# Kernel tuning notes

Hardware: AMD Instinct MI355X
Metric: run time of the kernel (lower is better)

Reference implementation:

```python
import jax, jax.numpy as jnp
import numpy as np

EPS = 1e-6
SKEL_ITERS = 10

def _minpool(x, kh, kw):
    # torch: -max_pool2d(-x) pads with +inf for the min
    return jax.lax.reduce_window(x, jnp.inf, jax.lax.min,
                                 (1, 1, kh, kw), (1, 1, 1, 1),
                                 ((0, 0), (0, 0), (kh // 2, kh // 2), (kw // 2, kw // 2)))

def _maxpool3(x):
    return jax.lax.reduce_window(x, -jnp.inf, jax.lax.max,
                                 (1, 1, 3, 3), (1, 1, 1, 1),
                                 ((0, 0), (0, 0), (1, 1), (1, 1)))

def soft_erode(img):
    return jnp.minimum(_minpool(img, 3, 1), _minpool(img, 1, 3))

def soft_open(img):
    return _maxpool3(soft_erode(img))

def soft_skeletonize(img, iterations=SKEL_ITERS):
    img = jnp.clip(img, 0.0, 1.0)
    skeleton = jax.nn.relu(img - soft_open(img))
    for _ in range(iterations):
        img = soft_erode(img)
        delta = jax.nn.relu(img - soft_open(img))
        skeleton = skeleton + jax.nn.relu(delta - skeleton * delta)
    return jnp.clip(skeleton, 0.0, 1.0)

def _bce_with_logits(x, t):
    # numerically stable elementwise BCE
    return jnp.maximum(x, 0.0) - x * t + jnp.log1p(jnp.exp(-jnp.abs(x)))

def binary_focal_loss_with_logits(logits, target, alpha=0.25, gamma=2.0):
    bce = _bce_with_logits(logits, target)
    probs = jax.nn.sigmoid(logits)
    p_t = probs * target + (1.0 - probs) * (1.0 - target)
    alpha_t = alpha * target + (1.0 - alpha) * (1.0 - target)
    return jnp.mean(alpha_t * (1.0 - p_t) ** gamma * bce)

def dice_loss_from_probs(pred, target, eps=EPS):
    p = pred.reshape(pred.shape[0], -1)
    t = target.reshape(target.shape[0], -1)
    inter = jnp.sum(p * t, axis=1)
    denom = jnp.sum(p, axis=1) + jnp.sum(t, axis=1)
    dice = (2.0 * inter + eps) / (denom + eps)
    return 1.0 - jnp.mean(dice)

def cldice_loss(pred_probs, target_probs, iterations=SKEL_ITERS, eps=EPS):
    ps = soft_skeletonize(pred_probs, iterations)
    ts = soft_skeletonize(target_probs, iterations)
    B = pred_probs.shape[0]
    prec = jnp.sum((ps * target_probs).reshape(B, -1), axis=1) / (jnp.sum(ps.reshape(B, -1), axis=1) + eps)
    sens = jnp.sum((ts * pred_probs).reshape(B, -1), axis=1) / (jnp.sum(ts.reshape(B, -1), axis=1) + eps)
    cl = (2.0 * prec * sens + eps) / (prec + sens + eps)
    return 1.0 - jnp.mean(cl)

def masked_smooth_l1(pred, target, mask):
    m = jnp.broadcast_to(mask, pred.shape)
    d = pred * m - target * m
    ad = jnp.abs(d)
    sl1 = jnp.where(ad < 1.0, 0.5 * d * d, ad - 0.5)
    msum = jnp.sum(m)
    loss = jnp.sum(sl1) / jnp.maximum(msum, 1.0)
    return jnp.where(msum == 0.0, 0.0, loss)

def setup_inputs() -> dict:
    key = jax.random.key(0)
    ks = jax.random.split(key, 12)
    shp = (8, 1, 512, 512)
    ashp = (8, 2, 512, 512)
    return {
        'mask_logits': jax.random.normal(ks[0], shp, jnp.float32),
        'skeleton_logits': jax.random.normal(ks[1], shp, jnp.float32),
        'uncertainty_logits': jax.random.normal(ks[2], shp, jnp.float32),
        'junction_logits': jax.random.normal(ks[3], shp, jnp.float32),
        'endpoint_logits': jax.random.normal(ks[4], shp, jnp.float32),
        'affinity_pred': jax.random.normal(ks[5], ashp, jnp.float32),
        'mask': jax.random.uniform(ks[6], shp, jnp.float32),
        'skeleton': jax.random.uniform(ks[7], shp, jnp.float32),
        'junction': jax.random.uniform(ks[8], shp, jnp.float32),
        'endpoint': jax.random.uniform(ks[9], shp, jnp.float32),
        'affinity_target': jax.random.normal(ks[10], ashp, jnp.float32),
        'uncertainty': jax.random.uniform(ks[11], shp, jnp.float32),
    }

def reference(mask_logits, skeleton_logits, uncertainty_logits, junction_logits,
              endpoint_logits, affinity_pred, mask, skeleton, junction, endpoint,
              affinity_target, uncertainty):
    mask_probs = jax.nn.sigmoid(mask_logits)
    skeleton_probs = jax.nn.sigmoid(skeleton_logits)
    uncertainty_probs = jax.nn.sigmoid(uncertainty_logits)

    mask_loss = dice_loss_from_probs(mask_probs, mask) + binary_focal_loss_with_logits(mask_logits, mask)
    skeleton_loss = dice_loss_from_probs(skeleton_probs, skeleton)
    topology_loss = cldice_loss(mask_probs, mask, iterations=SKEL_ITERS)
    node_loss = 0.5 * (binary_focal_loss_with_logits(junction_logits, junction) +
                       binary_focal_loss_with_logits(endpoint_logits, endpoint))
    affinity_loss = masked_smooth_l1(affinity_pred, affinity_target, skeleton)
    uncertainty_loss = jnp.mean((uncertainty_probs - uncertainty) ** 2)

    total = (1.0 * mask_loss + 1.0 * skeleton_loss + 0.5 * topology_loss +
             0.5 * node_loss + 0.5 * affinity_loss + 0.1 * uncertainty_loss)
    return total
```

## Files before the change

kernel.cpp:

```cpp
#include <hip/hip_runtime.h>
#include <math.h>

#define HH 512
#define WW 512
#define BATCH 8
#define PIX (HH * WW)
#define NCH 16
#define NPIX_TOT (NCH * PIX)
#define N_ELEM (BATCH * PIX)
#define EPSV 1e-6

#define ACC_COUNT 128
#define ACC_BYTES (ACC_COUNT * sizeof(double))
#define NPART 12
#define MRB 2048

__device__ __forceinline__ float sigm(float x) {
    return __fdividef(1.0f, 1.0f + __expf(-x));
}
__device__ __forceinline__ float clamp01(float v) { return fminf(fmaxf(v, 0.0f), 1.0f); }

__device__ __forceinline__ float focal_term(float x, float t, float p) {
    float bce = fmaxf(x, 0.0f) - x * t - __logf(fmaxf(p, 1.0f - p));
    float p_t = p * t + (1.0f - p) * (1.0f - t);
    float a_t = 0.25f * t + 0.75f * (1.0f - t);
    float om  = 1.0f - p_t;
    return a_t * om * om * bce;
}

__device__ __forceinline__ double blockReduceSum(double v, double* sm4) {
    int lane = threadIdx.x & 63, wid = threadIdx.x >> 6;
#pragma unroll
    for (int off = 32; off; off >>= 1) v += __shfl_down(v, off);
    __syncthreads();
    if (lane == 0) sm4[wid] = v;
    __syncthreads();
    double r = 0.0;
    if (threadIdx.x == 0) r = sm4[0] + sm4[1] + sm4[2] + sm4[3];
    return r;
}

struct F8 { float4 a, b; };

__device__ __forceinline__ float4 f4min(float4 x, float4 y) {
    return make_float4(fminf(x.x,y.x), fminf(x.y,y.y), fminf(x.z,y.z), fminf(x.w,y.w));
}
__device__ __forceinline__ float4 f4max(float4 x, float4 y) {
    return make_float4(fmaxf(x.x,y.x), fmaxf(x.y,y.y), fmaxf(x.z,y.z), fmaxf(x.w,y.w));
}
__device__ __forceinline__ F8 f8min(F8 x, F8 y) { F8 r; r.a=f4min(x.a,y.a); r.b=f4min(x.b,y.b); return r; }
__device__ __forceinline__ F8 f8max(F8 x, F8 y) { F8 r; r.a=f4max(x.a,y.a); r.b=f4max(x.b,y.b); return r; }
__device__ __forceinline__ F8 f8const(float v) {
    F8 r; r.a = make_float4(v,v,v,v); r.b = r.a; return r;
}
__device__ __forceinline__ F8 f8sigm(F8 x) {
    F8 r;
    r.a = make_float4(sigm(x.a.x), sigm(x.a.y), sigm(x.a.z), sigm(x.a.w));
    r.b = make_float4(sigm(x.b.x), sigm(x.b.y), sigm(x.b.z), sigm(x.b.w));
    return r;
}
__device__ __forceinline__ F8 f8clamp01(F8 x) {
    F8 r;
    r.a = make_float4(clamp01(x.a.x), clamp01(x.a.y), clamp01(x.a.z), clamp01(x.a.w));
    r.b = make_float4(clamp01(x.b.x), clamp01(x.b.y), clamp01(x.b.z), clamp01(x.b.w));
    return r;
}

__device__ __forceinline__ F8 erode_row(const F8& up, const F8& ce, const F8& dn, int lane) {
    F8 vm = f8min(f8min(up, dn), ce);
    float Lin = __shfl_up(ce.b.w, 1);
    float Rin = __shfl_down(ce.a.x, 1);
    if (lane == 0)  Lin = INFINITY;
    if (lane == 63) Rin = INFINITY;
    float4 la = make_float4(Lin,    ce.a.x, ce.a.y, ce.a.z);
    float4 lb = make_float4(ce.a.w, ce.b.x, ce.b.y, ce.b.z);
    float4 ra = make_float4(ce.a.y, ce.a.z, ce.a.w, ce.b.x);
    float4 rb = make_float4(ce.b.y, ce.b.z, ce.b.w, Rin);
    F8 r;
    r.a = f4min(vm.a, f4min(la, ra));
    r.b = f4min(vm.b, f4min(lb, rb));
    return r;
}

__device__ __forceinline__ F8 max3_row(const F8& u, const F8& c, const F8& d, int lane) {
    F8 vm = f8max(f8max(u, d), c);
    float Lin = __shfl_up(vm.b.w, 1);
    float Rin = __shfl_down(vm.a.x, 1);
    if (lane == 0)  Lin = -INFINITY;
    if (lane == 63) Rin = -INFINITY;
    float4 la = make_float4(Lin,    vm.a.x, vm.a.y, vm.a.z);
    float4 lb = make_float4(vm.a.w, vm.b.x, vm.b.y, vm.b.z);
    float4 ra = make_float4(vm.a.y, vm.a.z, vm.a.w, vm.b.x);
    float4 rb = make_float4(vm.b.y, vm.b.z, vm.b.w, Rin);
    F8 r;
    r.a = f4max(vm.a, f4max(la, ra));
    r.b = f4max(vm.b, f4max(lb, rb));
    return r;
}

__device__ __forceinline__ float4 f4updt(float4 t, float4 im, float4 mx) {
    return make_float4(t.x * (1.0f - fmaxf(im.x - mx.x, 0.0f)),
                       t.y * (1.0f - fmaxf(im.y - mx.y, 0.0f)),
                       t.z * (1.0f - fmaxf(im.z - mx.z, 0.0f)),
                       t.w * (1.0f - fmaxf(im.w - mx.w, 0.0f)));
}

template<int ITERS, int MODE>
__global__ __launch_bounds__(256, 2) void k_skel_engine(
    const float* __restrict__ srcA,
    const float* __restrict__ srcB,
    const float* __restrict__ mlg,
    const float* __restrict__ msk,
    float* __restrict__ imgOut,
    float* __restrict__ tOut,
    double* __restrict__ acc)
{
    __shared__ float xbuf[4][4][WW];
    __shared__ double sm4[4];

    const int tid   = threadIdx.x;
    const int lane  = tid & 63;
    const int w     = tid >> 6;
    const int c     = blockIdx.x >> 5;
    const int strip = blockIdx.x & 31;
    const int S     = strip * 16;
    const int grow0 = S - 8 + w * 8;
    const int x0    = lane * 8;
    const bool hasT = (w == 1 || w == 2);

    F8 img[8], t8[8];

#pragma unroll
    for (int j = 0; j < 8; ++j) {
        int g = grow0 + j;
        if (g < 0 || g >= HH) { img[j] = f8const(INFINITY); continue; }
        const float* base;
        if (MODE == 0) base = (c < 8) ? srcA + c * PIX : srcB + (c - 8) * PIX;
        else           base = srcA + c * PIX;
        const float* rp = base + (g << 9) + x0;
        F8 v; v.a = *(const float4*)rp; v.b = *(const float4*)(rp + 4);
        if (MODE == 0) v = (c < 8) ? f8sigm(v) : f8clamp01(v);
        img[j] = v;
    }
    if (MODE == 0) {
#pragma unroll
        for (int j = 0; j < 8; ++j) t8[j] = f8const(1.0f);
    } else {
        if (hasT) {
#pragma unroll
            for (int j = 0; j < 8; ++j) {
                const float* tp = srcB + c * PIX + ((grow0 + j) << 9) + x0;
                t8[j].a = *(const float4*)tp; t8[j].b = *(const float4*)(tp + 4);
            }
        } else {
#pragma unroll
            for (int j = 0; j < 8; ++j) t8[j] = f8const(1.0f);
        }
    }

    for (int it = 0; it < ITERS; ++it) {
        __syncthreads();
        *(float4*)&xbuf[w][0][x0]     = img[0].a;
        *(float4*)&xbuf[w][0][x0 + 4] = img[0].b;
        *(float4*)&xbuf[w][1][x0]     = img[1].a;
        *(float4*)&xbuf[w][1][x0 + 4] = img[1].b;
        *(float4*)&xbuf[w][2][x0]     = img[6].a;
        *(float4*)&xbuf[w][2][x0 + 4] = img[6].b;
        *(float4*)&xbuf[w][3][x0]     = img[7].a;
        *(float4*)&xbuf[w][3][x0 + 4] = img[7].b;
        __syncthreads();

        F8 hU0, hU1, hD0, hD1;
        if (w > 0) {
            hU0.a = *(float4*)&xbuf[w-1][2][x0]; hU0.b = *(float4*)&xbuf[w-1][2][x0 + 4];
            hU1.a = *(float4*)&xbuf[w-1][3][x0]; hU1.b = *(float4*)&xbuf[w-1][3][x0 + 4];
        } else { hU0 = f8const(INFINITY); hU1 = f8const(INFINITY); }
        if (w < 3) {
            hD0.a = *(float4*)&xbuf[w+1][0][x0]; hD0.b = *(float4*)&xbuf[w+1][0][x0 + 4];
            hD1.a = *(float4*)&xbuf[w+1][1][x0]; hD1.b = *(float4*)&xbuf[w+1][1][x0 + 4];
        } else { hD0 = f8const(INFINITY); hD1 = f8const(INFINITY); }

        F8 Em1 = erode_row(hU0, hU1, img[0], lane);
        { int g = grow0 - 1; if (g < 0 || g >= HH) Em1 = f8const(-INFINITY); }
        F8 E0  = erode_row(hU1, img[0], img[1], lane);
        { int g = grow0;     if (g < 0 || g >= HH) E0  = f8const(-INFINITY); }

#pragma unroll
        for (int j = 0; j < 8; ++j) {
            F8 ce = (j < 7) ? img[j + 1] : hD0;
            F8 dn = (j < 6) ? img[j + 2] : ((j == 6) ? hD0 : hD1);
            F8 Ep1 = erode_row(img[j], ce, dn, lane);
            { int g = grow0 + j + 1; if (g < 0 || g >= HH) Ep1 = f8const(-INFINITY); }
            if (hasT) {
                F8 mx = max3_row(Em1, E0, Ep1, lane);
                t8[j].a = f4updt(t8[j].a, img[j].a, mx.a);
                t8[j].b = f4updt(t8[j].b, img[j].b, mx.b);
            }
            img[j] = E0;
            Em1 = E0; E0 = Ep1;
        }
    }

    if (MODE == 0) {
        if (hasT) {
#pragma unroll
            for (int j = 0; j < 8; ++j) {
                int g = grow0 + j;
                float* ip = imgOut + c * PIX + (g << 9) + x0;
                *(float4*)ip       = img[j].a;
                *(float4*)(ip + 4) = img[j].b;
                float* tp = tOut + c * PIX + (g << 9) + x0;
                *(float4*)tp       = t8[j].a;
                *(float4*)(tp + 4) = t8[j].b;
            }
        }
    } else {
        double s0 = 0.0, s1 = 0.0;
        if (hasT) {
#pragma unroll
            for (int j = 0; j < 8; ++j) {
                int g = grow0 + j;
                const float* op = (c < 8) ? (msk + c * PIX + (g << 9) + x0)
                                          : (mlg + (c - 8) * PIX + (g << 9) + x0);
                F8 o; o.a = *(const float4*)op; o.b = *(const float4*)(op + 4);
                if (c >= 8) o = f8sigm(o);
                float ps0 = clamp01(1.0f - t8[j].a.x), ps1 = clamp01(1.0f - t8[j].a.y);
                float ps2 = clamp01(1.0f - t8[j].a.z), ps3 = clamp01(1.0f - t8[j].a.w);
                float ps4 = clamp01(1.0f - t8[j].b.x), ps5 = clamp01(1.0f - t8[j].b.y);
                float ps6 = clamp01(1.0f - t8[j].b.z), ps7 = clamp01(1.0f - t8[j].b.w);
                float rs = ((ps0 + ps1) + (ps2 + ps3)) + ((ps4 + ps5) + (ps6 + ps7));
                float rp = ((ps0 * o.a.x + ps1 * o.a.y) + (ps2 * o.a.z + ps3 * o.a.w))
                         + ((ps4 * o.b.x + ps5 * o.b.y) + (ps6 * o.b.z + ps7 * o.b.w));
                s1 += (double)rs;
                s0 += (double)rp;
            }
        }
        double r0 = blockReduceSum(s0, sm4);
        double r1 = blockReduceSum(s1, sm4);
        if (tid == 0) {
            if (c < 8) { atomicAdd(&acc[53 + c], r0);     atomicAdd(&acc[61 + c], r1); }
            else       { atomicAdd(&acc[69 + c - 8], r0); atomicAdd(&acc[77 + c - 8], r1); }
        }
    }
}

__global__ __launch_bounds__(256) void k_main_reduce(
    const float* __restrict__ mask_logits, const float* __restrict__ skel_logits,
    const float* __restrict__ unc_logits,  const float* __restrict__ junc_logits,
    const float* __restrict__ endp_logits, const float* __restrict__ aff_pred,
    const float* __restrict__ mask,        const float* __restrict__ skel,
    const float* __restrict__ junc,        const float* __restrict__ endp,
    const float* __restrict__ aff_tgt,     const float* __restrict__ unc,
    double* __restrict__ part)
{
    __shared__ double sm4[4];
    const int b   = blockIdx.x >> 8;
    const int pix = (blockIdx.x & 255) * 1024 + threadIdx.x * 4;
    const int i   = b * PIX + pix;

    float q0 = 0, q1 = 0, q2 = 0, q3 = 0, q4 = 0, q5 = 0;
    float q6 = 0, q7 = 0, q8 = 0, q9 = 0, q10 = 0;

    float4 ml = *(const float4*)&mask_logits[i];
    float4 mm = *(const float4*)&mask[i];
    float4 sl = *(const float4*)&skel_logits[i];
    float4 ss = *(const float4*)&skel[i];
    float4 jl = *(const float4*)&junc_logits[i];
    float4 jt = *(const float4*)&junc[i];
    float4 el = *(const float4*)&endp_logits[i];
    float4 et = *(const float4*)&endp[i];
    float4 ul = *(const float4*)&unc_logits[i];
    float4 ut = *(const float4*)&unc[i];
    float4 a0 = *(const float4*)&aff_pred[(b * 2 + 0) * PIX + pix];
    float4 t0 = *(const float4*)&aff_tgt [(b * 2 + 0) * PIX + pix];
    float4 a1 = *(const float4*)&aff_pred[(b * 2 + 1) * PIX + pix];
    float4 t1 = *(const float4*)&aff_tgt [(b * 2 + 1) * PIX + pix];

    const float* mlv = (const float*)&ml; const float* mmv = (const float*)&mm;
    const float* slv = (const float*)&sl; const float* ssv = (const float*)&ss;
    const float* jlv = (const float*)&jl; const float* jtv = (const float*)&jt;
    const float* elv = (const float*)&el; const float* etv = (const float*)&et;
    const float* ulv = (const float*)&ul; const float* utv = (const float*)&ut;
    const float* a0v = (const float*)&a0; const float* t0v = (const float*)&t0;
    const float* a1v = (const float*)&a1; const float* t1v = (const float*)&t1;

#pragma unroll
    for (int k = 0; k < 4; ++k) {
        float x = mlv[k], m = mmv[k];
        float p = sigm(x);
        q0 += p * m; q1 += p; q2 += m;
        q6 += focal_term(x, m, p);

        float sx = slv[k], s = ssv[k];
        float sp = sigm(sx);
        q3 += sp * s; q4 += sp; q5 += s;

        float jx = jlv[k];
        q7 += focal_term(jx, jtv[k], sigm(jx));
        float ex = elv[k];
        q8 += focal_term(ex, etv[k], sigm(ex));

        float ud = sigm(ulv[k]) - utv[k];
        q10 += ud * ud;

        float d0 = a0v[k] * s - t0v[k] * s;
        float ad0 = fabsf(d0);
        q9 += (ad0 < 1.0f) ? 0.5f * d0 * d0 : ad0 - 0.5f;
        float d1 = a1v[k] * s - t1v[k] * s;
        float ad1 = fabsf(d1);
        q9 += (ad1 < 1.0f) ? 0.5f * d1 * d1 : ad1 - 0.5f;
    }

    double* p = &part[blockIdx.x * NPART];
    double r;
    r = blockReduceSum((double)q0, sm4);  if (threadIdx.x == 0) p[0]  = r;
    r = blockReduceSum((double)q1, sm4);  if (threadIdx.x == 0) p[1]  = r;
    r = blockReduceSum((double)q2, sm4);  if (threadIdx.x == 0) p[2]  = r;
    r = blockReduceSum((double)q3, sm4);  if (threadIdx.x == 0) p[3]  = r;
    r = blockReduceSum((double)q4, sm4);  if (threadIdx.x == 0) p[4]  = r;
    r = blockReduceSum((double)q5, sm4);  if (threadIdx.x == 0) p[5]  = r;
    r = blockReduceSum((double)q6, sm4);  if (threadIdx.x == 0) p[6]  = r;
    r = blockReduceSum((double)q7, sm4);  if (threadIdx.x == 0) p[7]  = r;
    r = blockReduceSum((double)q8, sm4);  if (threadIdx.x == 0) p[8]  = r;
    r = blockReduceSum((double)q9, sm4);  if (threadIdx.x == 0) p[9]  = r;
    r = blockReduceSum((double)q10, sm4); if (threadIdx.x == 0) p[10] = r;
}

__global__ __launch_bounds__(256) void k_combine(
    const double* __restrict__ part, double* __restrict__ acc)
{
    const int wave = threadIdx.x >> 6, lane = threadIdx.x & 63;
    for (int T = wave; T < 53; T += 4) {
        double v = 0.0;
        if (T < 48) {
            int g = T >> 3, bb = T & 7;
            int blk = bb * 256 + lane * 4;
#pragma unroll
            for (int i = 0; i < 4; ++i) v += part[(blk + i) * NPART + g];
        } else {
            int q = 6 + (T - 48);
#pragma unroll
            for (int i = 0; i < 32; ++i) v += part[(lane + 64 * i) * NPART + q];
        }
#pragma unroll
        for (int off = 32; off; off >>= 1) v += __shfl_down(v, off);
        if (lane == 0) {
            if (T < 48) acc[(T >> 3) * 8 + (T & 7)] = v;
            else        acc[48 + (T - 48)] = v;
        }
    }
}

__global__ void k_finalize(const double* __restrict__ acc, float* __restrict__ out)
{
    if (threadIdx.x != 0 || blockIdx.x != 0) return;
    const double eps = EPSV;
    const double Nd  = (double)N_ELEM;

    double dm = 0, ds = 0, cl = 0, msum = 0;
    for (int b = 0; b < BATCH; ++b) {
        dm += (2.0 * acc[0 + b] + eps) / (acc[8 + b] + acc[16 + b] + eps);
        ds += (2.0 * acc[24 + b] + eps) / (acc[32 + b] + acc[40 + b] + eps);
        double prec = acc[53 + b] / (acc[61 + b] + eps);
        double sens = acc[69 + b] / (acc[77 + b] + eps);
        cl += (2.0 * prec * sens + eps) / (prec + sens + eps);
        msum += acc[40 + b];
    }
    msum *= 2.0;

    double mask_loss = (1.0 - dm / 8.0) + acc[48] / Nd;
    double skel_loss = 1.0 - ds / 8.0;
    double topo      = 1.0 - cl / 8.0;
    double node      = 0.5 * (acc[49] / Nd + acc[50] / Nd);
    double aff       = (msum == 0.0) ? 0.0 : acc[51] / fmax(msum, 1.0);
    double unc       = acc[52] / Nd;

    double total = mask_loss + skel_loss + 0.5 * topo + 0.5 * node + 0.5 * aff + 0.1 * unc;
    out[0] = (float)total;
}

extern "C" void kernel_launch(void* const* d_in, const int* in_sizes, int n_in,
                              void* d_out, int out_size, void* d_ws, size_t ws_size,
                              hipStream_t stream)
{
    const float* mask_logits = (const float*)d_in[0];
    const float* skel_logits = (const float*)d_in[1];
    const float* unc_logits  = (const float*)d_in[2];
    const float* junc_logits = (const float*)d_in[3];
    const float* endp_logits = (const float*)d_in[4];
    const float* aff_pred    = (const float*)d_in[5];
    const float* mask        = (const float*)d_in[6];
    const float* skel        = (const float*)d_in[7];
    const float* junc        = (const float*)d_in[8];
    const float* endp        = (const float*)d_in[9];
    const float* aff_tgt     = (const float*)d_in[10];
    const float* unc         = (const float*)d_in[11];
    float* out = (float*)d_out;

    char* ws = (char*)d_ws;
    double* acc  = (double*)ws;
    double* part = (double*)(ws + ACC_BYTES);
    float*  P1   = (float*)(ws + ACC_BYTES + MRB * NPART * sizeof(double));
    float*  TBUF = P1 + NPIX_TOT;

    hipMemsetAsync(acc, 0, ACC_BYTES, stream);

    k_main_reduce<<<MRB, 256, 0, stream>>>(
        mask_logits, skel_logits, unc_logits, junc_logits, endp_logits,
        aff_pred, mask, skel, junc, endp, aff_tgt, unc, part);
    k_combine<<<1, 256, 0, stream>>>(part, acc);

    k_skel_engine<6, 0><<<NCH * 32, 256, 0, stream>>>(
        mask_logits, mask, nullptr, nullptr, P1, TBUF, nullptr);
    k_skel_engine<5, 1><<<NCH * 32, 256, 0, stream>>>(
        P1, TBUF, mask_logits, mask, nullptr, nullptr, acc);

    k_finalize<<<1, 64, 0, stream>>>(acc, out);
}
```

Before: 243.9 us.

## Double-buffer skeleton halo LDS, batch reductions, and fold combine into finalize

```diff
diff --git a/kernel.cpp b/kernel.cpp
--- a/kernel.cpp
+++ b/kernel.cpp
@@ -13,7 +13,7 @@
 #define ACC_COUNT 128
 #define ACC_BYTES (ACC_COUNT * sizeof(double))
 #define NPART 12
-#define MRB 2048
+#define MRB 1024
 
 __device__ __forceinline__ float sigm(float x) {
     return __fdividef(1.0f, 1.0f + __expf(-x));
@@ -115,7 +115,7 @@
     float* __restrict__ tOut,
     double* __restrict__ acc)
 {
-    __shared__ float xbuf[4][4][WW];
+    __shared__ float xbuf[2][4][4][WW];
     __shared__ double sm4[4];
 
     const int tid   = threadIdx.x;
@@ -159,25 +159,25 @@
     }
 
     for (int it = 0; it < ITERS; ++it) {
-        __syncthreads();
-        *(float4*)&xbuf[w][0][x0]     = img[0].a;
-        *(float4*)&xbuf[w][0][x0 + 4] = img[0].b;
-        *(float4*)&xbuf[w][1][x0]     = img[1].a;
-        *(float4*)&xbuf[w][1][x0 + 4] = img[1].b;
-        *(float4*)&xbuf[w][2][x0]     = img[6].a;
-        *(float4*)&xbuf[w][2][x0 + 4] = img[6].b;
-        *(float4*)&xbuf[w][3][x0]     = img[7].a;
-        *(float4*)&xbuf[w][3][x0 + 4] = img[7].b;
+        const int pb = it & 1;
+        *(float4*)&xbuf[pb][w][0][x0]     = img[0].a;
+        *(float4*)&xbuf[pb][w][0][x0 + 4] = img[0].b;
+        *(float4*)&xbuf[pb][w][1][x0]     = img[1].a;
+        *(float4*)&xbuf[pb][w][1][x0 + 4] = img[1].b;
+        *(float4*)&xbuf[pb][w][2][x0]     = img[6].a;
+        *(float4*)&xbuf[pb][w][2][x0 + 4] = img[6].b;
+        *(float4*)&xbuf[pb][w][3][x0]     = img[7].a;
+        *(float4*)&xbuf[pb][w][3][x0 + 4] = img[7].b;
         __syncthreads();
 
         F8 hU0, hU1, hD0, hD1;
         if (w > 0) {
-            hU0.a = *(float4*)&xbuf[w-1][2][x0]; hU0.b = *(float4*)&xbuf[w-1][2][x0 + 4];
-            hU1.a = *(float4*)&xbuf[w-1][3][x0]; hU1.b = *(float4*)&xbuf[w-1][3][x0 + 4];
+            hU0.a = *(float4*)&xbuf[pb][w-1][2][x0]; hU0.b = *(float4*)&xbuf[pb][w-1][2][x0 + 4];
+            hU1.a = *(float4*)&xbuf[pb][w-1][3][x0]; hU1.b = *(float4*)&xbuf[pb][w-1][3][x0 + 4];
         } else { hU0 = f8const(INFINITY); hU1 = f8const(INFINITY); }
         if (w < 3) {
-            hD0.a = *(float4*)&xbuf[w+1][0][x0]; hD0.b = *(float4*)&xbuf[w+1][0][x0 + 4];
-            hD1.a = *(float4*)&xbuf[w+1][1][x0]; hD1.b = *(float4*)&xbuf[w+1][1][x0 + 4];
+            hD0.a = *(float4*)&xbuf[pb][w+1][0][x0]; hD0.b = *(float4*)&xbuf[pb][w+1][0][x0 + 4];
+            hD1.a = *(float4*)&xbuf[pb][w+1][1][x0]; hD1.b = *(float4*)&xbuf[pb][w+1][1][x0 + 4];
         } else { hD0 = f8const(INFINITY); hD1 = f8const(INFINITY); }
 
         F8 Em1 = erode_row(hU0, hU1, img[0], lane);
@@ -235,6 +235,7 @@
                 s0 += (double)rp;
             }
         }
+        __syncthreads();
         double r0 = blockReduceSum(s0, sm4);
         double r1 = blockReduceSum(s1, sm4);
         if (tid == 0) {
@@ -253,127 +254,134 @@
     const float* __restrict__ aff_tgt,     const float* __restrict__ unc,
     double* __restrict__ part)
 {
-    __shared__ double sm4[4];
-    const int b   = blockIdx.x >> 8;
-    const int pix = (blockIdx.x & 255) * 1024 + threadIdx.x * 4;
-    const int i   = b * PIX + pix;
-
-    float q0 = 0, q1 = 0, q2 = 0, q3 = 0, q4 = 0, q5 = 0;
-    float q6 = 0, q7 = 0, q8 = 0, q9 = 0, q10 = 0;
-
-    float4 ml = *(const float4*)&mask_logits[i];
-    float4 mm = *(const float4*)&mask[i];
-    float4 sl = *(const float4*)&skel_logits[i];
-    float4 ss = *(const float4*)&skel[i];
-    float4 jl = *(const float4*)&junc_logits[i];
-    float4 jt = *(const float4*)&junc[i];
-    float4 el = *(const float4*)&endp_logits[i];
-    float4 et = *(const float4*)&endp[i];
-    float4 ul = *(const float4*)&unc_logits[i];
-    float4 ut = *(const float4*)&unc[i];
-    float4 a0 = *(const float4*)&aff_pred[(b * 2 + 0) * PIX + pix];
-    float4 t0 = *(const float4*)&aff_tgt [(b * 2 + 0) * PIX + pix];
-    float4 a1 = *(const float4*)&aff_pred[(b * 2 + 1) * PIX + pix];
-    float4 t1 = *(const float4*)&aff_tgt [(b * 2 + 1) * PIX + pix];
-
-    const float* mlv = (const float*)&ml; const float* mmv = (const float*)&mm;
-    const float* slv = (const float*)&sl; const float* ssv = (const float*)&ss;
-    const float* jlv = (const float*)&jl; const float* jtv = (const float*)&jt;
-    const float* elv = (const float*)&el; const float* etv = (const float*)&et;
-    const float* ulv = (const float*)&ul; const float* utv = (const float*)&ut;
-    const float* a0v = (const float*)&a0; const float* t0v = (const float*)&t0;
-    const float* a1v = (const float*)&a1; const float* t1v = (const float*)&t1;
-
-#pragma unroll
-    for (int k = 0; k < 4; ++k) {
-        float x = mlv[k], m = mmv[k];
-        float p = sigm(x);
-        q0 += p * m; q1 += p; q2 += m;
-        q6 += focal_term(x, m, p);
-
-        float sx = slv[k], s = ssv[k];
-        float sp = sigm(sx);
-        q3 += sp * s; q4 += sp; q5 += s;
-
-        float jx = jlv[k];
-        q7 += focal_term(jx, jtv[k], sigm(jx));
-        float ex = elv[k];
-        q8 += focal_term(ex, etv[k], sigm(ex));
-
-        float ud = sigm(ulv[k]) - utv[k];
-        q10 += ud * ud;
-
-        float d0 = a0v[k] * s - t0v[k] * s;
-        float ad0 = fabsf(d0);
-        q9 += (ad0 < 1.0f) ? 0.5f * d0 * d0 : ad0 - 0.5f;
-        float d1 = a1v[k] * s - t1v[k] * s;
-        float ad1 = fabsf(d1);
-        q9 += (ad1 < 1.0f) ? 0.5f * d1 * d1 : ad1 - 0.5f;
-    }
-
-    double* p = &part[blockIdx.x * NPART];
-    double r;
-    r = blockReduceSum((double)q0, sm4);  if (threadIdx.x == 0) p[0]  = r;
-    r = blockReduceSum((double)q1, sm4);  if (threadIdx.x == 0) p[1]  = r;
-    r = blockReduceSum((double)q2, sm4);  if (threadIdx.x == 0) p[2]  = r;
-    r = blockReduceSum((double)q3, sm4);  if (threadIdx.x == 0) p[3]  = r;
-    r = blockReduceSum((double)q4, sm4);  if (threadIdx.x == 0) p[4]  = r;
-    r = blockReduceSum((double)q5, sm4);  if (threadIdx.x == 0) p[5]  = r;
-    r = blockReduceSum((double)q6, sm4);  if (threadIdx.x == 0) p[6]  = r;
-    r = blockReduceSum((double)q7, sm4);  if (threadIdx.x == 0) p[7]  = r;
-    r = blockReduceSum((double)q8, sm4);  if (threadIdx.x == 0) p[8]  = r;
-    r = blockReduceSum((double)q9, sm4);  if (threadIdx.x == 0) p[9]  = r;
-    r = blockReduceSum((double)q10, sm4); if (threadIdx.x == 0) p[10] = r;
-}
-
-__global__ __launch_bounds__(256) void k_combine(
-    const double* __restrict__ part, double* __restrict__ acc)
+    __shared__ float smq[4][11];
+    const int b    = blockIdx.x >> 7;
+    const int pix0 = (blockIdx.x & 127) * 2048;
+
+    float q[11];
+#pragma unroll
+    for (int i = 0; i < 11; ++i) q[i] = 0.0f;
+
+#pragma unroll 1
+    for (int r = 0; r < 2; ++r) {
+        const int pix = pix0 + r * 1024 + threadIdx.x * 4;
+        const int i   = b * PIX + pix;
+
+        float4 ml = *(const float4*)&mask_logits[i];
+        float4 mm = *(const float4*)&mask[i];
+        float4 sl = *(const float4*)&skel_logits[i];
+        float4 ss = *(const float4*)&skel[i];
+        float4 jl = *(const float4*)&junc_logits[i];
+        float4 jt = *(const float4*)&junc[i];
+        float4 el = *(const float4*)&endp_logits[i];
+        float4 et = *(const float4*)&endp[i];
+        float4 ul = *(const float4*)&unc_logits[i];
+        float4 ut = *(const float4*)&unc[i];
+        float4 a0 = *(const float4*)&aff_pred[(b * 2 + 0) * PIX + pix];
+        float4 t0 = *(const float4*)&aff_tgt [(b * 2 + 0) * PIX + pix];
+        float4 a1 = *(const float4*)&aff_pred[(b * 2 + 1) * PIX + pix];
+        float4 t1 = *(const float4*)&aff_tgt [(b * 2 + 1) * PIX + pix];
+
+        const float* mlv = (const float*)&ml; const float* mmv = (const float*)&mm;
+        const float* slv = (const float*)&sl; const float* ssv = (const float*)&ss;
+        const float* jlv = (const float*)&jl; const float* jtv = (const float*)&jt;
+        const float* elv = (const float*)&el; const float* etv = (const float*)&et;
+        const float* ulv = (const float*)&ul; const float* utv = (const float*)&ut;
+        const float* a0v = (const float*)&a0; const float* t0v = (const float*)&t0;
+        const float* a1v = (const float*)&a1; const float* t1v = (const float*)&t1;
+
+#pragma unroll
+        for (int k = 0; k < 4; ++k) {
+            float x = mlv[k], m = mmv[k];
+            float p = sigm(x);
+            q[0] += p * m; q[1] += p; q[2] += m;
+            q[6] += focal_term(x, m, p);
+
+            float sx = slv[k], s = ssv[k];
+            float sp = sigm(sx);
+            q[3] += sp * s; q[4] += sp; q[5] += s;
+
+            float jx = jlv[k];
+            q[7] += focal_term(jx, jtv[k], sigm(jx));
+            float ex = elv[k];
+            q[8] += focal_term(ex, etv[k], sigm(ex));
+
+            float ud = sigm(ulv[k]) - utv[k];
+            q[10] += ud * ud;
+
+            float d0 = a0v[k] * s - t0v[k] * s;
+            float ad0 = fabsf(d0);
+            q[9] += (ad0 < 1.0f) ? 0.5f * d0 * d0 : ad0 - 0.5f;
+            float d1 = a1v[k] * s - t1v[k] * s;
+            float ad1 = fabsf(d1);
+            q[9] += (ad1 < 1.0f) ? 0.5f * d1 * d1 : ad1 - 0.5f;
+        }
+    }
+
+#pragma unroll
+    for (int i = 0; i < 11; ++i) {
+        float v = q[i];
+        v += __shfl_xor(v, 1);  v += __shfl_xor(v, 2);  v += __shfl_xor(v, 4);
+        v += __shfl_xor(v, 8);  v += __shfl_xor(v, 16); v += __shfl_xor(v, 32);
+        q[i] = v;
+    }
+    const int lane = threadIdx.x & 63, wid = threadIdx.x >> 6;
+    if (lane == 0) {
+#pragma unroll
+        for (int i = 0; i < 11; ++i) smq[wid][i] = q[i];
+    }
+    __syncthreads();
+    if (threadIdx.x < 11) {
+        double v = (double)smq[0][threadIdx.x] + (double)smq[1][threadIdx.x]
+                 + (double)smq[2][threadIdx.x] + (double)smq[3][threadIdx.x];
+        part[blockIdx.x * NPART + threadIdx.x] = v;
+    }
+}
+
+__global__ __launch_bounds__(256) void k_finalize(
+    const double* __restrict__ part, const double* __restrict__ acc,
+    float* __restrict__ out)
 {
+    __shared__ double s[53];
     const int wave = threadIdx.x >> 6, lane = threadIdx.x & 63;
     for (int T = wave; T < 53; T += 4) {
         double v = 0.0;
         if (T < 48) {
             int g = T >> 3, bb = T & 7;
-            int blk = bb * 256 + lane * 4;
-#pragma unroll
-            for (int i = 0; i < 4; ++i) v += part[(blk + i) * NPART + g];
+            int blk = bb * 128 + lane * 2;
+            v = part[blk * NPART + g] + part[(blk + 1) * NPART + g];
         } else {
             int q = 6 + (T - 48);
 #pragma unroll
-            for (int i = 0; i < 32; ++i) v += part[(lane + 64 * i) * NPART + q];
+            for (int i = 0; i < 16; ++i) v += part[(lane + 64 * i) * NPART + q];
         }
 #pragma unroll
         for (int off = 32; off; off >>= 1) v += __shfl_down(v, off);
-        if (lane == 0) {
-            if (T < 48) acc[(T >> 3) * 8 + (T & 7)] = v;
-            else        acc[48 + (T - 48)] = v;
-        }
-    }
-}
-
-__global__ void k_finalize(const double* __restrict__ acc, float* __restrict__ out)
-{
-    if (threadIdx.x != 0 || blockIdx.x != 0) return;
+        if (lane == 0) s[T] = v;
+    }
+    __syncthreads();
+
+    if (threadIdx.x != 0) return;
     const double eps = EPSV;
     const double Nd  = (double)N_ELEM;
 
     double dm = 0, ds = 0, cl = 0, msum = 0;
     for (int b = 0; b < BATCH; ++b) {
-        dm += (2.0 * acc[0 + b] + eps) / (acc[8 + b] + acc[16 + b] + eps);
-        ds += (2.0 * acc[24 + b] + eps) / (acc[32 + b] + acc[40 + b] + eps);
+        dm += (2.0 * s[0 + b] + eps) / (s[8 + b] + s[16 + b] + eps);
+        ds += (2.0 * s[24 + b] + eps) / (s[32 + b] + s[40 + b] + eps);
         double prec = acc[53 + b] / (acc[61 + b] + eps);
         double sens = acc[69 + b] / (acc[77 + b] + eps);
         cl += (2.0 * prec * sens + eps) / (prec + sens + eps);
-        msum += acc[40 + b];
+        msum += s[40 + b];
     }
     msum *= 2.0;
 
-    double mask_loss = (1.0 - dm / 8.0) + acc[48] / Nd;
+    double mask_loss = (1.0 - dm / 8.0) + s[48] / Nd;
     double skel_loss = 1.0 - ds / 8.0;
     double topo      = 1.0 - cl / 8.0;
-    double node      = 0.5 * (acc[49] / Nd + acc[50] / Nd);
-    double aff       = (msum == 0.0) ? 0.0 : acc[51] / fmax(msum, 1.0);
-    double unc       = acc[52] / Nd;
+    double node      = 0.5 * (s[49] / Nd + s[50] / Nd);
+    double aff       = (msum == 0.0) ? 0.0 : s[51] / fmax(msum, 1.0);
+    double unc       = s[52] / Nd;
 
     double total = mask_loss + skel_loss + 0.5 * topo + 0.5 * node + 0.5 * aff + 0.1 * unc;
     out[0] = (float)total;
@@ -408,12 +416,11 @@
     k_main_reduce<<<MRB, 256, 0, stream>>>(
         mask_logits, skel_logits, unc_logits, junc_logits, endp_logits,
         aff_pred, mask, skel, junc, endp, aff_tgt, unc, part);
-    k_combine<<<1, 256, 0, stream>>>(part, acc);
 
     k_skel_engine<6, 0><<<NCH * 32, 256, 0, stream>>>(
         mask_logits, mask, nullptr, nullptr, P1, TBUF, nullptr);
     k_skel_engine<5, 1><<<NCH * 32, 256, 0, stream>>>(
         P1, TBUF, mask_logits, mask, nullptr, nullptr, acc);
 
-    k_finalize<<<1, 64, 0, stream>>>(acc, out);
-}
+    k_finalize<<<1, 256, 0, stream>>>(part, acc, out);
+}
```

Measured after the change: 230.4 us. 5.5% less time.
